# Optimization experiments

Measured on AMD Instinct MI355X. Metric: run time of the kernel, lower is better.

The kernel has to match this reference:

```python
import jax, jax.numpy as jnp
import numpy as np

RX, RY, RZ = 32, 32, 32
NORMALIZE = True
EPS = 0.0


def setup_inputs() -> dict:
    key = jax.random.key(0)
    k1, k2 = jax.random.split(key)
    features = jax.random.normal(k1, (16, 64, 65536), dtype=jnp.float32)  # [B, C, N]
    coords = jax.random.normal(k2, (16, 3, 65536), dtype=jnp.float32)     # [B, 3, N]
    return {"features": features, "coords": coords}


def _norm_and_voxel_coords(coords):
    # coords: [B, 3, N]
    nc = coords - coords.mean(axis=2, keepdims=True)
    if NORMALIZE:
        # per-point L2 norm over xyz (dim 1), max over points (dim 2)
        norm = jnp.linalg.norm(nc, axis=1, keepdims=True)            # [B, 1, N]
        denom = norm.max(axis=2, keepdims=True) * 2.0 + EPS          # [B, 1, 1]
        nc = nc / denom + 0.5
    else:
        nc = (nc + 1.0) / 2.0
    r = jnp.array([RX, RY, RZ], dtype=nc.dtype).reshape(1, 3, 1)
    nc = jnp.clip(nc * r, 0.0, r - 1.0)                              # per-axis clamp
    vox = jnp.round(nc).astype(jnp.int32)                            # [B, 3, N]
    return vox, nc


def _avg_voxelize(features, vox):
    # features: [B, C, N], vox: [B, 3, N] int32 -> [B, C, RX, RY, RZ]
    B, C, N = features.shape
    R = RX * RY * RZ
    idx = vox[:, 0] * (RY * RZ) + vox[:, 1] * RZ + vox[:, 2]          # [B, N]
    flat_idx = (idx + jnp.arange(B, dtype=jnp.int32)[:, None] * R).reshape(-1)  # [B*N]
    feats = features.transpose(0, 2, 1).reshape(B * N, C)             # [B*N, C]
    sums = jax.ops.segment_sum(feats, flat_idx, num_segments=B * R)   # [B*R, C]
    cnts = jax.ops.segment_sum(jnp.ones((B * N,), features.dtype), flat_idx,
                               num_segments=B * R)                    # [B*R]
    avg = sums / jnp.maximum(cnts, 1.0)[:, None]
    return avg.reshape(B, RX, RY, RZ, C).transpose(0, 4, 1, 2, 3)


def reference(features, coords):
    vox, norm_coords = _norm_and_voxel_coords(coords)
    out = _avg_voxelize(features, vox)
    return out, norm_coords
```

## Files before the change

### kernel.cpp

```cpp
#include <hip/hip_runtime.h>

#define BATCH 16
#define CH 64
#define NPTS 65536
#define RX 32
#define RY 32
#define RZ 32
#define RVOX (RX * RY * RZ)
#define HALFVOX (RVOX / 2)
#define NQ (NPTS / 4)

__global__ void mean_kernel(const float* __restrict__ coords, double* __restrict__ meanAcc) {
    const int b = blockIdx.y;
    const int t = blockIdx.x * blockDim.x + threadIdx.x;
    const float4* cb = (const float4*)(coords + (size_t)b * 3 * NPTS);
    double s[3];
#pragma unroll
    for (int d = 0; d < 3; ++d) {
        const float4 v = cb[d * NQ + t];
        s[d] = ((double)v.x + (double)v.y) + ((double)v.z + (double)v.w);
    }
#pragma unroll
    for (int off = 32; off > 0; off >>= 1) {
        s[0] += __shfl_down(s[0], off);
        s[1] += __shfl_down(s[1], off);
        s[2] += __shfl_down(s[2], off);
    }
    __shared__ double red[3][4];
    const int wave = threadIdx.x >> 6, lane = threadIdx.x & 63;
    if (lane == 0) { red[0][wave] = s[0]; red[1][wave] = s[1]; red[2][wave] = s[2]; }
    __syncthreads();
    if (threadIdx.x == 0) {
        double tx = 0, ty = 0, tz = 0;
        for (int w = 0; w < 4; ++w) { tx += red[0][w]; ty += red[1][w]; tz += red[2][w]; }
        atomicAdd(&meanAcc[b * 3 + 0], tx);
        atomicAdd(&meanAcc[b * 3 + 1], ty);
        atomicAdd(&meanAcc[b * 3 + 2], tz);
    }
}

__global__ void maxnorm_kernel(const float* __restrict__ coords,
                               const double* __restrict__ meanAcc,
                               int* __restrict__ maxAcc) {
    const int b = blockIdx.y;
    const int t = blockIdx.x * blockDim.x + threadIdx.x;
    const float4* cb = (const float4*)(coords + (size_t)b * 3 * NPTS);
    const float mx = (float)(meanAcc[b * 3 + 0] * (1.0 / NPTS));
    const float my = (float)(meanAcc[b * 3 + 1] * (1.0 / NPTS));
    const float mz = (float)(meanAcc[b * 3 + 2] * (1.0 / NPTS));
    const float4 x = cb[0 * NQ + t];
    const float4 y = cb[1 * NQ + t];
    const float4 z = cb[2 * NQ + t];
    float m = 0.0f;
    {
        float dx = x.x - mx, dy = y.x - my, dz = z.x - mz; m = fmaxf(m, dx*dx + dy*dy + dz*dz);
        dx = x.y - mx; dy = y.y - my; dz = z.y - mz;      m = fmaxf(m, dx*dx + dy*dy + dz*dz);
        dx = x.z - mx; dy = y.z - my; dz = z.z - mz;      m = fmaxf(m, dx*dx + dy*dy + dz*dz);
        dx = x.w - mx; dy = y.w - my; dz = z.w - mz;      m = fmaxf(m, dx*dx + dy*dy + dz*dz);
    }
#pragma unroll
    for (int off = 32; off > 0; off >>= 1) m = fmaxf(m, __shfl_down(m, off));
    __shared__ float redm[4];
    const int wave = threadIdx.x >> 6, lane = threadIdx.x & 63;
    if (lane == 0) redm[wave] = m;
    __syncthreads();
    if (threadIdx.x == 0) {
        float tmax = fmaxf(fmaxf(redm[0], redm[1]), fmaxf(redm[2], redm[3]));
        atomicMax(&maxAcc[b], __float_as_int(tmax));
    }
}

__global__ void point_kernel(const float* __restrict__ coords,
                             const double* __restrict__ meanAcc,
                             const int* __restrict__ maxAcc,
                             float* __restrict__ normc,
                             unsigned short* __restrict__ idx16,
                             float* __restrict__ counts) {
    const int t = blockIdx.x * blockDim.x + threadIdx.x;
    const int b = t >> 14;
    const int q = t & (NQ - 1);
    const float denom = 2.0f * sqrtf(__int_as_float(maxAcc[b]));
    const float4* cb = (const float4*)(coords + (size_t)b * 3 * NPTS);
    float4* nb = (float4*)(normc + (size_t)b * 3 * NPTS);
    int vx[3][4];
#pragma unroll
    for (int d = 0; d < 3; ++d) {
        const float m = (float)(meanAcc[b * 3 + d] * (1.0 / NPTS));
        float4 v = cb[d * NQ + q];
        float4 s;
        s.x = fminf(fmaxf(((v.x - m) / denom + 0.5f) * 32.0f, 0.0f), 31.0f);
        s.y = fminf(fmaxf(((v.y - m) / denom + 0.5f) * 32.0f, 0.0f), 31.0f);
        s.z = fminf(fmaxf(((v.z - m) / denom + 0.5f) * 32.0f, 0.0f), 31.0f);
        s.w = fminf(fmaxf(((v.w - m) / denom + 0.5f) * 32.0f, 0.0f), 31.0f);
        nb[d * NQ + q] = s;
        vx[d][0] = (int)rintf(s.x);
        vx[d][1] = (int)rintf(s.y);
        vx[d][2] = (int)rintf(s.z);
        vx[d][3] = (int)rintf(s.w);
    }
    ushort4 o;
    o.x = (unsigned short)(vx[0][0] * (RY * RZ) + vx[1][0] * RZ + vx[2][0]);
    o.y = (unsigned short)(vx[0][1] * (RY * RZ) + vx[1][1] * RZ + vx[2][1]);
    o.z = (unsigned short)(vx[0][2] * (RY * RZ) + vx[1][2] * RZ + vx[2][2]);
    o.w = (unsigned short)(vx[0][3] * (RY * RZ) + vx[1][3] * RZ + vx[2][3]);
    ((ushort4*)(idx16 + (size_t)b * NPTS))[q] = o;
    float* cbp = counts + (size_t)b * RVOX;
    atomicAdd(&cbp[o.x], 1.0f);
    atomicAdd(&cbp[o.y], 1.0f);
    atomicAdd(&cbp[o.z], 1.0f);
    atomicAdd(&cbp[o.w], 1.0f);
}

__global__ __launch_bounds__(1024) void accum_kernel(const float* __restrict__ features,
                                                     const unsigned short* __restrict__ idx16,
                                                     const float* __restrict__ counts,
                                                     float* __restrict__ out) {
    __shared__ float g[HALFVOX];
    const int c = blockIdx.x;
    const int b = blockIdx.y;
    const int tid = threadIdx.x;
    const float4* fs = (const float4*)(features + ((size_t)(b * CH + c)) * NPTS);
    const ushort4* is = (const ushort4*)(idx16 + (size_t)b * NPTS);
    const float* cb = counts + (size_t)b * RVOX;
    float* ob = out + ((size_t)(b * CH + c)) * RVOX;

#pragma unroll
    for (int half = 0; half < 2; ++half) {
        for (int i = tid; i < HALFVOX; i += 1024) g[i] = 0.0f;
        __syncthreads();
        const unsigned short want = (unsigned short)half;
        for (int base = tid; base < NQ; base += 4096) {
            const float4 f0 = fs[base];
            const float4 f1 = fs[base + 1024];
            const float4 f2 = fs[base + 2048];
            const float4 f3 = fs[base + 3072];
            const ushort4 v0 = is[base];
            const ushort4 v1 = is[base + 1024];
            const ushort4 v2 = is[base + 2048];
            const ushort4 v3 = is[base + 3072];
            if ((v0.x >> 14) == want) atomicAdd(&g[v0.x & (HALFVOX - 1)], f0.x);
            if ((v0.y >> 14) == want) atomicAdd(&g[v0.y & (HALFVOX - 1)], f0.y);
            if ((v0.z >> 14) == want) atomicAdd(&g[v0.z & (HALFVOX - 1)], f0.z);
            if ((v0.w >> 14) == want) atomicAdd(&g[v0.w & (HALFVOX - 1)], f0.w);
            if ((v1.x >> 14) == want) atomicAdd(&g[v1.x & (HALFVOX - 1)], f1.x);
            if ((v1.y >> 14) == want) atomicAdd(&g[v1.y & (HALFVOX - 1)], f1.y);
            if ((v1.z >> 14) == want) atomicAdd(&g[v1.z & (HALFVOX - 1)], f1.z);
            if ((v1.w >> 14) == want) atomicAdd(&g[v1.w & (HALFVOX - 1)], f1.w);
            if ((v2.x >> 14) == want) atomicAdd(&g[v2.x & (HALFVOX - 1)], f2.x);
            if ((v2.y >> 14) == want) atomicAdd(&g[v2.y & (HALFVOX - 1)], f2.y);
            if ((v2.z >> 14) == want) atomicAdd(&g[v2.z & (HALFVOX - 1)], f2.z);
            if ((v2.w >> 14) == want) atomicAdd(&g[v2.w & (HALFVOX - 1)], f2.w);
            if ((v3.x >> 14) == want) atomicAdd(&g[v3.x & (HALFVOX - 1)], f3.x);
            if ((v3.y >> 14) == want) atomicAdd(&g[v3.y & (HALFVOX - 1)], f3.y);
            if ((v3.z >> 14) == want) atomicAdd(&g[v3.z & (HALFVOX - 1)], f3.z);
            if ((v3.w >> 14) == want) atomicAdd(&g[v3.w & (HALFVOX - 1)], f3.w);
        }
        __syncthreads();
        const float* ch = cb + half * HALFVOX;
        float* oh = ob + half * HALFVOX;
        for (int i = tid; i < HALFVOX / 4; i += 1024) {
            const float4 c4 = ((const float4*)ch)[i];
            float4 v = ((const float4*)g)[i];
            v.x /= fmaxf(c4.x, 1.0f);
            v.y /= fmaxf(c4.y, 1.0f);
            v.z /= fmaxf(c4.z, 1.0f);
            v.w /= fmaxf(c4.w, 1.0f);
            ((float4*)oh)[i] = v;
        }
        __syncthreads();
    }
}

extern "C" void kernel_launch(void* const* d_in, const int* in_sizes, int n_in,
                              void* d_out, int out_size, void* d_ws, size_t ws_size,
                              hipStream_t stream) {
    const float* features = (const float*)d_in[0];
    const float* coords = (const float*)d_in[1];
    float* out = (float*)d_out;
    float* normc = out + (size_t)BATCH * CH * RVOX;

    char* ws = (char*)d_ws;
    double* meanAcc = (double*)ws;
    int* maxAcc = (int*)(ws + 384);
    float* counts = (float*)(ws + 512);
    unsigned short* idx16 = (unsigned short*)(ws + 512 + (size_t)BATCH * RVOX * 4);

    hipMemsetAsync(ws, 0, 512 + (size_t)BATCH * RVOX * 4, stream);

    dim3 gred(NQ / 256, BATCH);
    mean_kernel<<<gred, 256, 0, stream>>>(coords, meanAcc);
    maxnorm_kernel<<<gred, 256, 0, stream>>>(coords, meanAcc, maxAcc);

    point_kernel<<<(BATCH * NQ) / 256, 256, 0, stream>>>(coords, meanAcc, maxAcc,
                                                         normc, idx16, counts);

    accum_kernel<<<dim3(CH, BATCH), 1024, 0, stream>>>(features, idx16, counts, out);
}
```

Measured before the change: 732.2 us.

## Replace per-channel shared-atomic voxelization with counting-sort scatter and segmented gather

The old approach read all points once per channel and did LDS atomics over two half-grid passes. The new code runs a prefix scan over the voxel counts, then scatters each point's 64-channel feature row into voxel-sorted order in a workspace buffer. A gather kernel then reduces contiguous runs per voxel block, with few atomics, and writes the normalized averages. This adds an extra write and read of the full feature array through the workspace, plus global atomics on a cursor, and it may need several batch chunks if the workspace is small.

Result: slower. 985.0 us (+34.5%).

```diff
diff --git a/kernel.cpp b/kernel.cpp
--- a/kernel.cpp
+++ b/kernel.cpp
@@ -7,7 +7,6 @@
 #define RY 32
 #define RZ 32
 #define RVOX (RX * RY * RZ)
-#define HALFVOX (RVOX / 2)
 #define NQ (NPTS / 4)
 
 __global__ void mean_kernel(const float* __restrict__ coords, double* __restrict__ meanAcc) {
@@ -111,63 +110,115 @@
     atomicAdd(&cbp[o.w], 1.0f);
 }
 
-__global__ __launch_bounds__(1024) void accum_kernel(const float* __restrict__ features,
-                                                     const unsigned short* __restrict__ idx16,
+__global__ __launch_bounds__(1024) void scan_kernel(const float* __restrict__ counts,
+                                                    int* __restrict__ offs,
+                                                    int* __restrict__ cursor) {
+    const int b = blockIdx.x;
+    const int tid = threadIdx.x;
+    const float4* cb = (const float4*)(counts + (size_t)b * RVOX);
+    int loc[32];
+    int sum = 0;
+#pragma unroll
+    for (int k8 = 0; k8 < 8; ++k8) {
+        const float4 c4 = cb[tid * 8 + k8];
+        loc[k8 * 4 + 0] = sum; sum += (int)c4.x;
+        loc[k8 * 4 + 1] = sum; sum += (int)c4.y;
+        loc[k8 * 4 + 2] = sum; sum += (int)c4.z;
+        loc[k8 * 4 + 3] = sum; sum += (int)c4.w;
+    }
+    int inc = sum;
+    const int lane = tid & 63;
+#pragma unroll
+    for (int off = 1; off < 64; off <<= 1) {
+        const int n = __shfl_up(inc, off);
+        if (lane >= off) inc += n;
+    }
+    __shared__ int wtot[16];
+    const int wid = tid >> 6;
+    if (lane == 63) wtot[wid] = inc;
+    __syncthreads();
+    if (tid == 0) {
+        int r = 0;
+        for (int w = 0; w < 16; ++w) { const int t = wtot[w]; wtot[w] = r; r += t; }
+    }
+    __syncthreads();
+    const int base = wtot[wid] + (inc - sum);
+    int* ob = offs + (size_t)b * RVOX + tid * 32;
+    int* ub = cursor + (size_t)b * RVOX + tid * 32;
+#pragma unroll
+    for (int k = 0; k < 32; ++k) { ob[k] = base + loc[k]; ub[k] = base + loc[k]; }
+}
+
+__global__ __launch_bounds__(256) void scatter_kernel(const float* __restrict__ features,
+                                                      const unsigned short* __restrict__ idx16,
+                                                      int* __restrict__ cursor,
+                                                      unsigned short* __restrict__ vsorted,
+                                                      float* __restrict__ ftb, int b0) {
+    const int b = b0 + blockIdx.y;
+    const int n0 = blockIdx.x * 128;
+    const int tid = threadIdx.x;
+    __shared__ float tile[128][65];
+    __shared__ int slots[128];
+    if (tid < 128) {
+        const int v = idx16[(size_t)b * NPTS + n0 + tid];
+        const int slot = atomicAdd(&cursor[(size_t)b * RVOX + v], 1);
+        slots[tid] = slot;
+        vsorted[(size_t)b * NPTS + slot] = (unsigned short)v;
+    }
+    const float* fb = features + ((size_t)b * CH) * NPTS + n0;
+    const int j = tid & 127;
+#pragma unroll
+    for (int cc = 0; cc < 32; ++cc) {
+        const int c = cc * 2 + (tid >> 7);
+        tile[j][c] = fb[(size_t)c * NPTS + j];
+    }
+    __syncthreads();
+    const int wid = tid >> 6, lane = tid & 63;
+    float* fout = ftb + ((size_t)(b - b0) * NPTS) * CH;
+    for (int p = wid * 32; p < wid * 32 + 32; ++p) {
+        fout[(size_t)slots[p] * CH + lane] = tile[p][lane];
+    }
+}
+
+__global__ __launch_bounds__(256) void gather_kernel(const float* __restrict__ ftb,
+                                                     const unsigned short* __restrict__ vsorted,
+                                                     const int* __restrict__ offs,
                                                      const float* __restrict__ counts,
-                                                     float* __restrict__ out) {
-    __shared__ float g[HALFVOX];
-    const int c = blockIdx.x;
-    const int b = blockIdx.y;
+                                                     float* __restrict__ out, int b0) {
+    const int b = b0 + blockIdx.y;
+    const int v0 = blockIdx.x * 64;
     const int tid = threadIdx.x;
-    const float4* fs = (const float4*)(features + ((size_t)(b * CH + c)) * NPTS);
-    const ushort4* is = (const ushort4*)(idx16 + (size_t)b * NPTS);
-    const float* cb = counts + (size_t)b * RVOX;
-    float* ob = out + ((size_t)(b * CH + c)) * RVOX;
-
-#pragma unroll
-    for (int half = 0; half < 2; ++half) {
-        for (int i = tid; i < HALFVOX; i += 1024) g[i] = 0.0f;
-        __syncthreads();
-        const unsigned short want = (unsigned short)half;
-        for (int base = tid; base < NQ; base += 4096) {
-            const float4 f0 = fs[base];
-            const float4 f1 = fs[base + 1024];
-            const float4 f2 = fs[base + 2048];
-            const float4 f3 = fs[base + 3072];
-            const ushort4 v0 = is[base];
-            const ushort4 v1 = is[base + 1024];
-            const ushort4 v2 = is[base + 2048];
-            const ushort4 v3 = is[base + 3072];
-            if ((v0.x >> 14) == want) atomicAdd(&g[v0.x & (HALFVOX - 1)], f0.x);
-            if ((v0.y >> 14) == want) atomicAdd(&g[v0.y & (HALFVOX - 1)], f0.y);
-            if ((v0.z >> 14) == want) atomicAdd(&g[v0.z & (HALFVOX - 1)], f0.z);
-            if ((v0.w >> 14) == want) atomicAdd(&g[v0.w & (HALFVOX - 1)], f0.w);
-            if ((v1.x >> 14) == want) atomicAdd(&g[v1.x & (HALFVOX - 1)], f1.x);
-            if ((v1.y >> 14) == want) atomicAdd(&g[v1.y & (HALFVOX - 1)], f1.y);
-            if ((v1.z >> 14) == want) atomicAdd(&g[v1.z & (HALFVOX - 1)], f1.z);
-            if ((v1.w >> 14) == want) atomicAdd(&g[v1.w & (HALFVOX - 1)], f1.w);
-            if ((v2.x >> 14) == want) atomicAdd(&g[v2.x & (HALFVOX - 1)], f2.x);
-            if ((v2.y >> 14) == want) atomicAdd(&g[v2.y & (HALFVOX - 1)], f2.y);
-            if ((v2.z >> 14) == want) atomicAdd(&g[v2.z & (HALFVOX - 1)], f2.z);
-            if ((v2.w >> 14) == want) atomicAdd(&g[v2.w & (HALFVOX - 1)], f2.w);
-            if ((v3.x >> 14) == want) atomicAdd(&g[v3.x & (HALFVOX - 1)], f3.x);
-            if ((v3.y >> 14) == want) atomicAdd(&g[v3.y & (HALFVOX - 1)], f3.y);
-            if ((v3.z >> 14) == want) atomicAdd(&g[v3.z & (HALFVOX - 1)], f3.z);
-            if ((v3.w >> 14) == want) atomicAdd(&g[v3.w & (HALFVOX - 1)], f3.w);
+    __shared__ float acc_t[64][65];
+    for (int i = tid; i < 64 * 65; i += 256) ((float*)acc_t)[i] = 0.0f;
+    __syncthreads();
+    const int pstart = offs[(size_t)b * RVOX + v0];
+    const int pend = (blockIdx.x == (RVOX / 64) - 1) ? NPTS
+                                                     : offs[(size_t)b * RVOX + v0 + 64];
+    const int wid = tid >> 6, lane = tid & 63;
+    const int len = pend - pstart;
+    const int s = pstart + ((len * wid) >> 2);
+    const int e = pstart + ((len * (wid + 1)) >> 2);
+    const unsigned short* vs = vsorted + (size_t)b * NPTS;
+    const float* fb = ftb + ((size_t)(b - b0) * NPTS) * CH;
+    float acc = 0.0f;
+    int vcur = -1;
+    for (int i = s; i < e; ++i) {
+        const float f = fb[(size_t)i * CH + lane];
+        const int vox = vs[i];
+        if (vox != vcur) {
+            if (vcur >= 0) atomicAdd(&acc_t[vcur - v0][lane], acc);
+            acc = 0.0f; vcur = vox;
         }
-        __syncthreads();
-        const float* ch = cb + half * HALFVOX;
-        float* oh = ob + half * HALFVOX;
-        for (int i = tid; i < HALFVOX / 4; i += 1024) {
-            const float4 c4 = ((const float4*)ch)[i];
-            float4 v = ((const float4*)g)[i];
-            v.x /= fmaxf(c4.x, 1.0f);
-            v.y /= fmaxf(c4.y, 1.0f);
-            v.z /= fmaxf(c4.z, 1.0f);
-            v.w /= fmaxf(c4.w, 1.0f);
-            ((float4*)oh)[i] = v;
-        }
-        __syncthreads();
+        acc += f;
+    }
+    if (vcur >= 0) atomicAdd(&acc_t[vcur - v0][lane], acc);
+    __syncthreads();
+    const float cnt = fmaxf(counts[(size_t)b * RVOX + v0 + lane], 1.0f);
+    float* ob = out + ((size_t)b * CH) * RVOX + v0;
+#pragma unroll
+    for (int k = 0; k < 16; ++k) {
+        const int c = k * 4 + wid;
+        ob[(size_t)c * RVOX + lane] = acc_t[lane][c] / cnt;
     }
 }
 
@@ -183,16 +234,34 @@
     double* meanAcc = (double*)ws;
     int* maxAcc = (int*)(ws + 384);
     float* counts = (float*)(ws + 512);
-    unsigned short* idx16 = (unsigned short*)(ws + 512 + (size_t)BATCH * RVOX * 4);
-
-    hipMemsetAsync(ws, 0, 512 + (size_t)BATCH * RVOX * 4, stream);
+    unsigned short* idx16 = (unsigned short*)(ws + 512 + 1 * 2097152);
+    int* offs = (int*)(ws + 512 + 2 * 2097152);
+    int* cursor = (int*)(ws + 512 + 3 * 2097152);
+    unsigned short* vsorted = (unsigned short*)(ws + 512 + 4 * 2097152);
+    float* ftb = (float*)(ws + 512 + 5 * 2097152);
+    const size_t fixed = 512 + 5 * (size_t)2097152;
+    const size_t per_batch = (size_t)NPTS * CH * 4;
+    int G = 1;
+    if (ws_size > fixed + per_batch) {
+        size_t g = (ws_size - fixed) / per_batch;
+        G = (g >= BATCH) ? BATCH : (int)g;
+        if (G < 1) G = 1;
+    }
+
+    hipMemsetAsync(ws, 0, 512 + 2097152, stream);
 
     dim3 gred(NQ / 256, BATCH);
     mean_kernel<<<gred, 256, 0, stream>>>(coords, meanAcc);
     maxnorm_kernel<<<gred, 256, 0, stream>>>(coords, meanAcc, maxAcc);
-
     point_kernel<<<(BATCH * NQ) / 256, 256, 0, stream>>>(coords, meanAcc, maxAcc,
                                                          normc, idx16, counts);
-
-    accum_kernel<<<dim3(CH, BATCH), 1024, 0, stream>>>(features, idx16, counts, out);
-}
+    scan_kernel<<<BATCH, 1024, 0, stream>>>(counts, offs, cursor);
+
+    for (int b0 = 0; b0 < BATCH; b0 += G) {
+        const int g = (BATCH - b0 < G) ? (BATCH - b0) : G;
+        scatter_kernel<<<dim3(NPTS / 128, g), 256, 0, stream>>>(features, idx16, cursor,
+                                                                vsorted, ftb, b0);
+        gather_kernel<<<dim3(RVOX / 64, g), 256, 0, stream>>>(ftb, vsorted, offs,
+                                                              counts, out, b0);
+    }
+}
```

## Replace shared-memory atomic scatter with counting-sort segmented reduction

Applied to the files above, without the earlier changes.

Builds a per-batch voxel histogram and prefix scan, then counting-sorts the points by voxel. Each point's 64-channel feature row is scattered into a point-major buffer in sorted order. Warps then run segmented sums over contiguous runs, and a transposing finalize kernel divides by counts. This replaces the two-pass per-channel LDS atomic accumulation, which reread the indices for every channel. In exchange it needs a large workspace (features plus voxel grid per batch group) and extra global traffic, and falls back to the old path when the workspace is too small.

New measurement: 613.5 us. 16.2% less time.

```diff
diff --git a/kernel.cpp b/kernel.cpp
--- a/kernel.cpp
+++ b/kernel.cpp
@@ -74,8 +74,7 @@
                              const double* __restrict__ meanAcc,
                              const int* __restrict__ maxAcc,
                              float* __restrict__ normc,
-                             unsigned short* __restrict__ idx16,
-                             float* __restrict__ counts) {
+                             unsigned short* __restrict__ idx16) {
     const int t = blockIdx.x * blockDim.x + threadIdx.x;
     const int b = t >> 14;
     const int q = t & (NQ - 1);
@@ -104,6 +103,174 @@
     o.z = (unsigned short)(vx[0][2] * (RY * RZ) + vx[1][2] * RZ + vx[2][2]);
     o.w = (unsigned short)(vx[0][3] * (RY * RZ) + vx[1][3] * RZ + vx[2][3]);
     ((ushort4*)(idx16 + (size_t)b * NPTS))[q] = o;
+}
+
+__global__ __launch_bounds__(1024) void histscan_kernel(const unsigned short* __restrict__ idx16,
+                                                        int* __restrict__ cursor,
+                                                        float* __restrict__ counts) {
+    const int b = blockIdx.x;
+    const int tid = threadIdx.x;
+    __shared__ unsigned int h32[RVOX / 2];
+#pragma unroll
+    for (int k = 0; k < RVOX / 2 / 1024; ++k) h32[tid + k * 1024] = 0u;
+    __syncthreads();
+    const ushort4* q = (const ushort4*)(idx16 + (size_t)b * NPTS);
+#pragma unroll
+    for (int k = 0; k < NPTS / 4 / 1024; ++k) {
+        const ushort4 v = q[tid + k * 1024];
+        atomicAdd(&h32[v.x >> 1], 1u << ((v.x & 1) * 16));
+        atomicAdd(&h32[v.y >> 1], 1u << ((v.y & 1) * 16));
+        atomicAdd(&h32[v.z >> 1], 1u << ((v.z & 1) * 16));
+        atomicAdd(&h32[v.w >> 1], 1u << ((v.w & 1) * 16));
+    }
+    __syncthreads();
+    int loc[32];
+    int cnt[32];
+    int sum = 0;
+#pragma unroll
+    for (int w = 0; w < 16; ++w) {
+        const unsigned pw = h32[tid * 16 + w];
+        const int c0 = (int)(pw & 0xffffu), c1 = (int)(pw >> 16);
+        loc[2 * w] = sum; cnt[2 * w] = c0; sum += c0;
+        loc[2 * w + 1] = sum; cnt[2 * w + 1] = c1; sum += c1;
+    }
+    int inc = sum;
+    const int lane = tid & 63;
+#pragma unroll
+    for (int off = 1; off < 64; off <<= 1) {
+        const int n = __shfl_up(inc, off);
+        if (lane >= off) inc += n;
+    }
+    __syncthreads();
+    int* wtot = (int*)h32;
+    const int wid = tid >> 6;
+    if (lane == 63) wtot[wid] = inc;
+    __syncthreads();
+    if (tid == 0) {
+        int r = 0;
+        for (int w = 0; w < 16; ++w) { const int t = wtot[w]; wtot[w] = r; r += t; }
+    }
+    __syncthreads();
+    const int base = wtot[wid] + (inc - sum);
+    int* ub = cursor + (size_t)b * RVOX + tid * 32;
+    float* cb = counts + (size_t)b * RVOX + tid * 32;
+#pragma unroll
+    for (int k = 0; k < 32; ++k) { ub[k] = base + loc[k]; cb[k] = (float)cnt[k]; }
+}
+
+__global__ __launch_bounds__(256) void scatter_kernel(const float* __restrict__ features,
+                                                      const unsigned short* __restrict__ idx16,
+                                                      int* __restrict__ cursor,
+                                                      unsigned short* __restrict__ vsorted,
+                                                      float* __restrict__ ftb, int b0) {
+    const int b = b0 + blockIdx.y;
+    const int n0 = blockIdx.x * 128;
+    const int tid = threadIdx.x;
+    __shared__ float tile[128][65];
+    __shared__ int slots[128];
+    if (tid < 128) {
+        const int v = idx16[(size_t)b * NPTS + n0 + tid];
+        const int slot = atomicAdd(&cursor[(size_t)b * RVOX + v], 1);
+        slots[tid] = slot;
+        vsorted[(size_t)b * NPTS + slot] = (unsigned short)v;
+    }
+    const float* fb = features + ((size_t)b * CH) * NPTS + n0;
+    const int j = tid & 127;
+#pragma unroll
+    for (int cc = 0; cc < 32; ++cc) {
+        const int c = cc * 2 + (tid >> 7);
+        tile[j][c] = fb[(size_t)c * NPTS + j];
+    }
+    __syncthreads();
+    const int wid = tid >> 6, lane = tid & 63;
+    float* fout = ftb + ((size_t)(b - b0) * NPTS) * CH;
+    for (int p = wid * 32; p < wid * 32 + 32; ++p) {
+        fout[(size_t)slots[p] * CH + lane] = tile[p][lane];
+    }
+}
+
+__global__ __launch_bounds__(256) void zero_boundary_kernel(const unsigned short* __restrict__ vsorted,
+                                                            float* __restrict__ acc, int b0) {
+    const int b = b0 + blockIdx.y;
+    const int tid = threadIdx.x;
+    const int wid = tid >> 6, lane = tid & 63;
+    const int slice = blockIdx.x * 4 + wid;
+    const unsigned short* vs = vsorted + (size_t)b * NPTS;
+    const int v1 = vs[slice * 256];
+    const int v2 = vs[slice * 256 + 255];
+    float* ab = acc + ((size_t)(b - b0) * RVOX) * CH;
+    ab[(size_t)v1 * CH + lane] = 0.0f;
+    ab[(size_t)v2 * CH + lane] = 0.0f;
+}
+
+__global__ __launch_bounds__(256) void gather_kernel(const float* __restrict__ ftb,
+                                                     const unsigned short* __restrict__ vsorted,
+                                                     float* __restrict__ acc, int b0) {
+    const int b = b0 + blockIdx.y;
+    const int tid = threadIdx.x;
+    const int wid = tid >> 6, lane = tid & 63;
+    const int slice = blockIdx.x * 4 + wid;
+    const int s = slice * 256;
+    const unsigned short* vs = vsorted + (size_t)b * NPTS;
+    const float* fb = ftb + ((size_t)(b - b0) * NPTS) * CH;
+    float* ab = acc + ((size_t)(b - b0) * RVOX) * CH;
+
+    int vcur = vs[s];
+    float a = 0.0f;
+    bool boundary = true;
+    for (int base = s; base < s + 256; base += 8) {
+        float f[8];
+        const uint4 vv = *(const uint4*)(vs + base);
+#pragma unroll
+        for (int k = 0; k < 8; ++k) f[k] = fb[(size_t)(base + k) * CH + lane];
+#pragma unroll
+        for (int k = 0; k < 8; ++k) {
+            const unsigned w = ((const unsigned*)&vv)[k >> 1];
+            const int v = (int)((w >> ((k & 1) * 16)) & 0xffffu);
+            if (v != vcur) {
+                if (boundary) { atomicAdd(&ab[(size_t)vcur * CH + lane], a); boundary = false; }
+                else          { ab[(size_t)vcur * CH + lane] = a; }
+                vcur = v; a = 0.0f;
+            }
+            a += f[k];
+        }
+    }
+    atomicAdd(&ab[(size_t)vcur * CH + lane], a);
+}
+
+__global__ __launch_bounds__(256) void finalize_kernel(const float* __restrict__ acc,
+                                                       const float* __restrict__ counts,
+                                                       float* __restrict__ out, int b0) {
+    const int b = b0 + blockIdx.y;
+    const int v0 = blockIdx.x * 64;
+    const int tid = threadIdx.x;
+    const int wid = tid >> 6, lane = tid & 63;
+    __shared__ float tile[64][65];
+    __shared__ float cvec[64];
+    if (tid < 64) cvec[tid] = counts[(size_t)b * RVOX + v0 + tid];
+    __syncthreads();
+    const float* ab = acc + ((size_t)(b - b0) * RVOX + v0) * CH;
+#pragma unroll
+    for (int k = 0; k < 16; ++k) {
+        const int row = k * 4 + wid;
+        tile[row][lane] = (cvec[row] > 0.0f) ? ab[(size_t)row * CH + lane] : 0.0f;
+    }
+    __syncthreads();
+    const float d = fmaxf(cvec[lane], 1.0f);
+    float* ob = out + ((size_t)b * CH) * RVOX + v0;
+#pragma unroll
+    for (int k = 0; k < 16; ++k) {
+        const int c = k * 4 + wid;
+        ob[(size_t)c * RVOX + lane] = tile[lane][c] / d;
+    }
+}
+
+__global__ void count_kernel(const unsigned short* __restrict__ idx16,
+                             float* __restrict__ counts) {
+    const int t = blockIdx.x * blockDim.x + threadIdx.x;
+    const int b = t >> 14;
+    const int q = t & (NQ - 1);
+    const ushort4 o = ((const ushort4*)(idx16 + (size_t)b * NPTS))[q];
     float* cbp = counts + (size_t)b * RVOX;
     atomicAdd(&cbp[o.x], 1.0f);
     atomicAdd(&cbp[o.y], 1.0f);
@@ -183,16 +350,45 @@
     double* meanAcc = (double*)ws;
     int* maxAcc = (int*)(ws + 384);
     float* counts = (float*)(ws + 512);
-    unsigned short* idx16 = (unsigned short*)(ws + 512 + (size_t)BATCH * RVOX * 4);
-
-    hipMemsetAsync(ws, 0, 512 + (size_t)BATCH * RVOX * 4, stream);
+    unsigned short* idx16 = (unsigned short*)(ws + 512 + 1 * 2097152);
+    int* cursor = (int*)(ws + 512 + 2 * 2097152);
+    unsigned short* vsorted = (unsigned short*)(ws + 512 + 3 * 2097152);
+    char* grpbase = ws + 512 + 4 * 2097152;
+    const size_t fixed = 512 + 4 * (size_t)2097152;
+    const size_t per_batch = (size_t)NPTS * CH * 4 + (size_t)RVOX * CH * 4;
+
+    int G = 0;
+    if (ws_size >= fixed + per_batch) {
+        size_t g = (ws_size - fixed) / per_batch;
+        G = (g >= BATCH) ? BATCH : (int)g;
+    }
 
     dim3 gred(NQ / 256, BATCH);
-    mean_kernel<<<gred, 256, 0, stream>>>(coords, meanAcc);
-    maxnorm_kernel<<<gred, 256, 0, stream>>>(coords, meanAcc, maxAcc);
-
-    point_kernel<<<(BATCH * NQ) / 256, 256, 0, stream>>>(coords, meanAcc, maxAcc,
-                                                         normc, idx16, counts);
-
-    accum_kernel<<<dim3(CH, BATCH), 1024, 0, stream>>>(features, idx16, counts, out);
-}
+
+    if (G >= 1) {
+        hipMemsetAsync(ws, 0, 512, stream);
+        mean_kernel<<<gred, 256, 0, stream>>>(coords, meanAcc);
+        maxnorm_kernel<<<gred, 256, 0, stream>>>(coords, meanAcc, maxAcc);
+        point_kernel<<<(BATCH * NQ) / 256, 256, 0, stream>>>(coords, meanAcc, maxAcc,
+                                                             normc, idx16);
+        histscan_kernel<<<BATCH, 1024, 0, stream>>>(idx16, cursor, counts);
+        for (int b0 = 0; b0 < BATCH; b0 += G) {
+            const int g = (BATCH - b0 < G) ? (BATCH - b0) : G;
+            float* ftb = (float*)grpbase;
+            float* acc = (float*)(grpbase + (size_t)g * NPTS * CH * 4);
+            scatter_kernel<<<dim3(NPTS / 128, g), 256, 0, stream>>>(features, idx16, cursor,
+                                                                    vsorted, ftb, b0);
+            zero_boundary_kernel<<<dim3(64, g), 256, 0, stream>>>(vsorted, acc, b0);
+            gather_kernel<<<dim3(64, g), 256, 0, stream>>>(ftb, vsorted, acc, b0);
+            finalize_kernel<<<dim3(RVOX / 64, g), 256, 0, stream>>>(acc, counts, out, b0);
+        }
+    } else {
+        hipMemsetAsync(ws, 0, 512 + 2097152, stream);
+        mean_kernel<<<gred, 256, 0, stream>>>(coords, meanAcc);
+        maxnorm_kernel<<<gred, 256, 0, stream>>>(coords, meanAcc, maxAcc);
+        point_kernel<<<(BATCH * NQ) / 256, 256, 0, stream>>>(coords, meanAcc, maxAcc,
+                                                             normc, idx16);
+        count_kernel<<<(BATCH * NQ) / 256, 256, 0, stream>>>(idx16, counts);
+        accum_kernel<<<dim3(CH, BATCH), 1024, 0, stream>>>(features, idx16, counts, out);
+    }
+}
```
